# Performance work log

Hardware: AMD Instinct MI355X
Metric: run time of the kernel (lower is better)

## Reference

```python
import jax, jax.numpy as jnp
import numpy as np
from jax import lax

NUM_WORDS, WORD_DIM = 50000, 300
NUM_CHARS, CHAR_DIM = 100, 100
NUM_POS, POS_DIM = 50, 100
NUM_FILTERS, KERNEL = 100, 3
PRIVACY_TERMS = (3, 7, 11)


def setup_inputs() -> dict:
    key = jax.random.key(0)
    ks = jax.random.split(key, 8)
    bs, ls, cl = 64, 512, 32
    return {
        "input_word": jax.random.randint(ks[0], (bs, ls), 0, NUM_WORDS, dtype=jnp.int64 if jax.config.jax_enable_x64 else jnp.int32),
        "input_char": jax.random.randint(ks[1], (bs, ls, cl), 0, NUM_CHARS),
        "input_pos": jax.random.randint(ks[2], (bs, ls), 0, NUM_POS),
        "word_table": jax.random.normal(ks[3], (NUM_WORDS, WORD_DIM), jnp.float32) * 0.1,
        "char_table": jax.random.normal(ks[4], (NUM_CHARS, CHAR_DIM), jnp.float32) * 0.1,
        "pos_table": jax.random.normal(ks[5], (NUM_POS, POS_DIM), jnp.float32) * 0.1,
        "conv_w": jax.random.normal(ks[6], (NUM_FILTERS, CHAR_DIM, KERNEL), jnp.float32) * 0.05,
        "conv_b": jax.random.normal(ks[7], (NUM_FILTERS,), jnp.float32) * 0.05,
    }


def _dist_feature(input_pos):
    # nearest-privacy-token distance: parallel prefix-min via cummax/cummin scans
    priv = jnp.asarray(PRIVACY_TERMS)
    pri_mask = (input_pos[..., None] == priv).any(-1)           # [bs, ls]
    ls = input_pos.shape[1]
    pos_idx = jnp.arange(ls)                                      # [ls]
    last = lax.cummax(jnp.where(pri_mask, pos_idx, -1000), axis=1)                 # last privacy idx <= j
    nxt = lax.cummin(jnp.where(pri_mask, pos_idx, 1000), axis=1, reverse=True)     # next privacy idx >= j
    dis = jnp.minimum(pos_idx - last, nxt - pos_idx).astype(jnp.float32)
    return dis[..., None]                                         # [bs, ls, 1]


def _char_cnn(char_emb, conv_w, conv_b):
    # char_emb: [bs, ls, cl, char_dim] -> [bs, ls, num_filters]
    bs, ls, cl, cd = char_emb.shape
    x = char_emb.reshape(bs * ls, cl, cd).transpose(0, 2, 1)      # [N, C, L]
    y = lax.conv_general_dilated(x, conv_w, window_strides=(1,),
                                 padding=[(KERNEL - 1, KERNEL - 1)],
                                 dimension_numbers=("NCH", "OIH", "NCH"))
    y = y + conv_b[None, :, None]
    y = jnp.tanh(y.max(axis=2))                                   # max over length, then tanh
    return y.reshape(bs, ls, -1)


def reference(input_word, input_char, input_pos, word_table, char_table, pos_table, conv_w, conv_b):
    dis = _dist_feature(input_pos)
    word = word_table[input_word]                                 # [bs, ls, word_dim]
    char = _char_cnn(char_table[input_char], conv_w, conv_b)      # [bs, ls, num_filters]
    pos = pos_table[input_pos]                                    # [bs, ls, pos_dim]
    return jnp.concatenate([dis, word, char, pos], axis=2)
```

## Files before the change

### kernel.cpp

```cpp
#include <hip/hip_runtime.h>
#include <hip/hip_fp16.h>

#define BS 64
#define LS 512
#define CL 32
#define WD 300
#define NC 100
#define CD 100
#define PD 100
#define NF 100
#define KK 3
#define OPAD 128
#define PROW (KK*OPAD)
#define PBYTES (NC*PROW*2)
#define NV4 (PBYTES/16)
#define OUTD 501
#define TPB 64
#define NTHR 1024

typedef _Float16 h2 __attribute__((ext_vector_type(2)));

__global__ void precompute_P(const float* __restrict__ conv_w,
                             const float* __restrict__ char_table,
                             _Float16* __restrict__ P) {
    const int c = blockIdx.x;
    const int k = blockIdx.y;
    const int o = threadIdx.x;
    __shared__ float row[CD];
    if (o < CD) row[o] = char_table[c * CD + o];
    __syncthreads();
    float acc = 0.f;
    if (o < NF) {
        const float* w = conv_w + o * (CD * KK) + k;
        #pragma unroll 4
        for (int i = 0; i < CD; ++i) acc += w[i * KK] * row[i];
    }
    P[(c * KK + k) * OPAD + o] = (_Float16)acc;
}

__global__ __launch_bounds__(NTHR, 8) void main_kernel(
        const int* __restrict__ input_word,
        const int* __restrict__ input_char,
        const int* __restrict__ input_pos,
        const float* __restrict__ word_table,
        const float* __restrict__ pos_table,
        const float* __restrict__ conv_b,
        const _Float16* __restrict__ Pg,
        float* __restrict__ out) {
    __shared__ alignas(16) _Float16 Pl[NC * PROW];
    __shared__ alignas(16) unsigned char s_char[TPB * CL];
    __shared__ unsigned long long s_mask[LS / 64];

    const int tid  = threadIdx.x;
    const int tok0 = blockIdx.x * TPB;

    const uint4* src = (const uint4*)Pg;
    const uint4 s0 = src[tid];
    const uint4 s1 = src[tid + NTHR];
    const uint4 s2 = src[tid + 2 * NTHR];
    const uint4 s3 = src[tid + 3 * NTHR];
    uint4 s4 = {};
    const bool h4 = tid < (NV4 - 4 * NTHR);
    if (h4) s4 = src[tid + 4 * NTHR];

    if (tid < LS) {
        const int p = input_pos[(tok0 >> 9) * LS + tid];
        const bool pm = (p == 3) | (p == 7) | (p == 11);
        const unsigned long long b = __ballot(pm);
        if ((tid & 63) == 0) s_mask[tid >> 6] = b;
    }

    if (tid < (TPB * CL) / 4) {
        const int4 c4 = ((const int4*)(input_char + tok0 * CL))[tid];
        ((unsigned*)s_char)[tid] =
            (unsigned)c4.x | ((unsigned)c4.y << 8) | ((unsigned)c4.z << 16) | ((unsigned)c4.w << 24);
    }

    {
        uint4* dst = (uint4*)Pl;
        dst[tid] = s0;
        dst[tid + NTHR] = s1;
        dst[tid + 2 * NTHR] = s2;
        dst[tid + 3 * NTHR] = s3;
        if (h4) dst[tid + 4 * NTHR] = s4;
    }
    __syncthreads();

    if (tid < 512) {
        const int wid  = tid >> 6;
        const int lane = tid & 63;
        const int l    = lane & 15;
        const char* Pb = (const char*)Pl + l * 16;
        const unsigned* s_cw = (const unsigned*)s_char;

        #pragma unroll 1
        for (int pass = 0; pass < 2; ++pass) {
            const int tb = wid * 8 + pass * 4 + (lane >> 4);
            h2 a0[4], a1[4], m[4];
            #pragma unroll
            for (int i = 0; i < 4; ++i) {
                a0[i] = (h2)(_Float16)0;
                a1[i] = (h2)(_Float16)0;
                m[i]  = (h2)(_Float16)(-60000.f);
            }
            #pragma unroll 2
            for (int w = 0; w < CL / 4; ++w) {
                const unsigned wd = s_cw[tb * (CL / 4) + w];
                #pragma unroll
                for (int b = 0; b < 4; ++b) {
                    const int ca = (int)((wd >> (8 * b)) & 0xFFu) * (PROW * 2);
                    const uint4 r0 = *(const uint4*)(Pb + ca + 0 * (OPAD * 2));
                    const uint4 r1 = *(const uint4*)(Pb + ca + 1 * (OPAD * 2));
                    const uint4 r2 = *(const uint4*)(Pb + ca + 2 * (OPAD * 2));
                    #pragma unroll
                    for (int i = 0; i < 4; ++i) {
                        const unsigned c0 = (i == 0) ? r0.x : (i == 1) ? r0.y : (i == 2) ? r0.z : r0.w;
                        const unsigned c1 = (i == 0) ? r1.x : (i == 1) ? r1.y : (i == 2) ? r1.z : r1.w;
                        const unsigned c2 = (i == 0) ? r2.x : (i == 1) ? r2.y : (i == 2) ? r2.z : r2.w;
                        const h2 p0 = __builtin_bit_cast(h2, c0);
                        const h2 p1 = __builtin_bit_cast(h2, c1);
                        const h2 p2 = __builtin_bit_cast(h2, c2);
                        const h2 y = a0[i] + p2;
                        m[i]  = __builtin_elementwise_max(m[i], y);
                        a0[i] = a1[i] + p1;
                        a1[i] = p0;
                    }
                }
            }
            if (l < 13) {
                float mm[8];
                #pragma unroll
                for (int i = 0; i < 4; ++i) {
                    const h2 v = __builtin_elementwise_max(m[i], __builtin_elementwise_max(a0[i], a1[i]));
                    mm[2 * i]     = (float)v.x;
                    mm[2 * i + 1] = (float)v.y;
                }
                const float4 b0 = *(const float4*)(conv_b + 8 * l);
                float* outc = out + (size_t)(tok0 + tb) * OUTD + 301 + 8 * l;
                outc[0] = tanhf(mm[0] + b0.x);
                outc[1] = tanhf(mm[1] + b0.y);
                outc[2] = tanhf(mm[2] + b0.z);
                outc[3] = tanhf(mm[3] + b0.w);
                if (l < 12) {
                    const float4 b1 = *(const float4*)(conv_b + 8 * l + 4);
                    outc[4] = tanhf(mm[4] + b1.x);
                    outc[5] = tanhf(mm[5] + b1.y);
                    outc[6] = tanhf(mm[6] + b1.z);
                    outc[7] = tanhf(mm[7] + b1.w);
                }
            }
        }
    } else {
        const int t2 = tid - 512;

        for (int i = t2; i < TPB * (WD / 4); i += 512) {
            const int t = i / (WD / 4);
            const int j = i - t * (WD / 4);
            const int w = input_word[tok0 + t];
            const float4 v = ((const float4*)word_table)[(size_t)w * (WD / 4) + j];
            float* o = out + (size_t)(tok0 + t) * OUTD + 1 + 4 * j;
            o[0] = v.x; o[1] = v.y; o[2] = v.z; o[3] = v.w;
        }
        for (int i = t2; i < TPB * (PD / 4); i += 512) {
            const int t = i / (PD / 4);
            const int j = i - t * (PD / 4);
            const int p = input_pos[tok0 + t];
            const float4 v = ((const float4*)pos_table)[p * (PD / 4) + j];
            float* o = out + (size_t)(tok0 + t) * OUTD + 401 + 4 * j;
            o[0] = v.x; o[1] = v.y; o[2] = v.z; o[3] = v.w;
        }
        if (t2 < TPB) {
            const int j = (tok0 & (LS - 1)) + t2;
            const int wj = j >> 6, bj = j & 63;
            int last = -1000;
            {
                unsigned long long x = s_mask[wj] & ((2ull << bj) - 1ull);
                int w = wj;
                while (true) {
                    if (x) { last = w * 64 + 63 - __clzll(x); break; }
                    if (--w < 0) break;
                    x = s_mask[w];
                }
            }
            int nxt = 1000;
            {
                unsigned long long x = s_mask[wj] & (~0ull << bj);
                int w = wj;
                while (true) {
                    if (x) { nxt = w * 64 + (int)__ffsll((long long)x) - 1; break; }
                    if (++w >= LS / 64) break;
                    x = s_mask[w];
                }
            }
            out[(size_t)(tok0 + t2) * OUTD] = (float)min(j - last, nxt - j);
        }
    }
}

extern "C" void kernel_launch(void* const* d_in, const int* in_sizes, int n_in,
                              void* d_out, int out_size, void* d_ws, size_t ws_size,
                              hipStream_t stream) {
    const int*   input_word = (const int*)d_in[0];
    const int*   input_char = (const int*)d_in[1];
    const int*   input_pos  = (const int*)d_in[2];
    const float* word_table = (const float*)d_in[3];
    const float* char_table = (const float*)d_in[4];
    const float* pos_table  = (const float*)d_in[5];
    const float* conv_w     = (const float*)d_in[6];
    const float* conv_b     = (const float*)d_in[7];
    float* out = (float*)d_out;

    _Float16* P = (_Float16*)d_ws;

    precompute_P<<<dim3(NC, KK), 128, 0, stream>>>(conv_w, char_table, P);
    main_kernel<<<(BS * LS) / TPB, NTHR, 0, stream>>>(
        input_word, input_char, input_pos, word_table, pos_table, conv_b, P, out);
}
```

Baseline: 38.90 us.

## Store char-conv projection table in FP8 and rebalance gather work across halves

The precomputed char-by-filter projection table is now quantized to FP8 (e4m3) instead of FP16. This halves the table's global-to-LDS copy and the per-character LDS reads, with a packed fp8-to-f32-to-f16 conversion added in the inner loop. The pos-embedding gather and distance feature move from the word-gather half of the block to the CNN half, and the word-gather loop is unrolled. FP8 quantization of the conv partial sums adds significant numerical error that may exceed tolerance, and the extra conversion instructions add ALU cost.

```diff
diff --git a/kernel.cpp b/kernel.cpp
--- a/kernel.cpp
+++ b/kernel.cpp
@@ -10,19 +10,26 @@
 #define PD 100
 #define NF 100
 #define KK 3
-#define OPAD 128
-#define PROW (KK*OPAD)
-#define PBYTES (NC*PROW*2)
-#define NV4 (PBYTES/16)
+#define OPAD8 128
+#define PROW8 (KK*OPAD8)
+#define PBYTES8 (NC*PROW8)
+#define NV4_8 (PBYTES8/16)
 #define OUTD 501
 #define TPB 64
 #define NTHR 1024
 
 typedef _Float16 h2 __attribute__((ext_vector_type(2)));
+typedef float f32x2 __attribute__((ext_vector_type(2)));
+
+template <bool HI>
+__device__ __forceinline__ h2 cvt2(unsigned w) {
+    f32x2 f = __builtin_amdgcn_cvt_pk_f32_fp8((int)w, HI);
+    return __builtin_bit_cast(h2, __builtin_amdgcn_cvt_pkrtz(f.x, f.y));
+}
 
 __global__ void precompute_P(const float* __restrict__ conv_w,
                              const float* __restrict__ char_table,
-                             _Float16* __restrict__ P) {
+                             unsigned char* __restrict__ P) {
     const int c = blockIdx.x;
     const int k = blockIdx.y;
     const int o = threadIdx.x;
@@ -35,8 +42,20 @@
         #pragma unroll 4
         for (int i = 0; i < CD; ++i) acc += w[i * KK] * row[i];
     }
-    P[(c * KK + k) * OPAD + o] = (_Float16)acc;
-}
+    const int enc = __builtin_amdgcn_cvt_pk_fp8_f32(acc, 0.f, 0, false);
+    P[(c * KK + k) * OPAD8 + o] = (unsigned char)(enc & 0xFF);
+}
+
+#define TAP(i, W0, W1, W2, HI)                                          \
+    {                                                                   \
+        const h2 p0 = cvt2<HI>(W0);                                     \
+        const h2 p1 = cvt2<HI>(W1);                                     \
+        const h2 p2 = cvt2<HI>(W2);                                     \
+        const h2 y = a0[i] + p2;                                        \
+        m[i]  = __builtin_elementwise_max(m[i], y);                     \
+        a0[i] = a1[i] + p1;                                             \
+        a1[i] = p0;                                                     \
+    }
 
 __global__ __launch_bounds__(NTHR, 8) void main_kernel(
         const int* __restrict__ input_word,
@@ -45,9 +64,9 @@
         const float* __restrict__ word_table,
         const float* __restrict__ pos_table,
         const float* __restrict__ conv_b,
-        const _Float16* __restrict__ Pg,
+        const unsigned char* __restrict__ Pg,
         float* __restrict__ out) {
-    __shared__ alignas(16) _Float16 Pl[NC * PROW];
+    __shared__ alignas(16) unsigned char Pl[PBYTES8];
     __shared__ alignas(16) unsigned char s_char[TPB * CL];
     __shared__ unsigned long long s_mask[LS / 64];
 
@@ -57,11 +76,9 @@
     const uint4* src = (const uint4*)Pg;
     const uint4 s0 = src[tid];
     const uint4 s1 = src[tid + NTHR];
-    const uint4 s2 = src[tid + 2 * NTHR];
-    const uint4 s3 = src[tid + 3 * NTHR];
-    uint4 s4 = {};
-    const bool h4 = tid < (NV4 - 4 * NTHR);
-    if (h4) s4 = src[tid + 4 * NTHR];
+    uint4 s2 = {};
+    const bool h2nd = tid < (NV4_8 - 2 * NTHR);
+    if (h2nd) s2 = src[tid + 2 * NTHR];
 
     if (tid < LS) {
         const int p = input_pos[(tok0 >> 9) * LS + tid];
@@ -80,9 +97,7 @@
         uint4* dst = (uint4*)Pl;
         dst[tid] = s0;
         dst[tid + NTHR] = s1;
-        dst[tid + 2 * NTHR] = s2;
-        dst[tid + 3 * NTHR] = s3;
-        if (h4) dst[tid + 4 * NTHR] = s4;
+        if (h2nd) dst[tid + 2 * NTHR] = s2;
     }
     __syncthreads();
 
@@ -90,7 +105,7 @@
         const int wid  = tid >> 6;
         const int lane = tid & 63;
         const int l    = lane & 15;
-        const char* Pb = (const char*)Pl + l * 16;
+        const char* Pb = (const char*)Pl + l * 8;
         const unsigned* s_cw = (const unsigned*)s_char;
 
         #pragma unroll 1
@@ -103,28 +118,19 @@
                 a1[i] = (h2)(_Float16)0;
                 m[i]  = (h2)(_Float16)(-60000.f);
             }
-            #pragma unroll 2
+            #pragma unroll 1
             for (int w = 0; w < CL / 4; ++w) {
                 const unsigned wd = s_cw[tb * (CL / 4) + w];
                 #pragma unroll
                 for (int b = 0; b < 4; ++b) {
-                    const int ca = (int)((wd >> (8 * b)) & 0xFFu) * (PROW * 2);
-                    const uint4 r0 = *(const uint4*)(Pb + ca + 0 * (OPAD * 2));
-                    const uint4 r1 = *(const uint4*)(Pb + ca + 1 * (OPAD * 2));
-                    const uint4 r2 = *(const uint4*)(Pb + ca + 2 * (OPAD * 2));
-                    #pragma unroll
-                    for (int i = 0; i < 4; ++i) {
-                        const unsigned c0 = (i == 0) ? r0.x : (i == 1) ? r0.y : (i == 2) ? r0.z : r0.w;
-                        const unsigned c1 = (i == 0) ? r1.x : (i == 1) ? r1.y : (i == 2) ? r1.z : r1.w;
-                        const unsigned c2 = (i == 0) ? r2.x : (i == 1) ? r2.y : (i == 2) ? r2.z : r2.w;
-                        const h2 p0 = __builtin_bit_cast(h2, c0);
-                        const h2 p1 = __builtin_bit_cast(h2, c1);
-                        const h2 p2 = __builtin_bit_cast(h2, c2);
-                        const h2 y = a0[i] + p2;
-                        m[i]  = __builtin_elementwise_max(m[i], y);
-                        a0[i] = a1[i] + p1;
-                        a1[i] = p0;
-                    }
+                    const int ca = (int)((wd >> (8 * b)) & 0xFFu) * PROW8;
+                    const uint2 q0 = *(const uint2*)(Pb + ca + 0 * OPAD8);
+                    const uint2 q1 = *(const uint2*)(Pb + ca + 1 * OPAD8);
+                    const uint2 q2 = *(const uint2*)(Pb + ca + 2 * OPAD8);
+                    TAP(0, q0.x, q1.x, q2.x, false)
+                    TAP(1, q0.x, q1.x, q2.x, true)
+                    TAP(2, q0.y, q1.y, q2.y, false)
+                    TAP(3, q0.y, q1.y, q2.y, true)
                 }
             }
             if (l < 13) {
@@ -150,18 +156,8 @@
                 }
             }
         }
-    } else {
-        const int t2 = tid - 512;
-
-        for (int i = t2; i < TPB * (WD / 4); i += 512) {
-            const int t = i / (WD / 4);
-            const int j = i - t * (WD / 4);
-            const int w = input_word[tok0 + t];
-            const float4 v = ((const float4*)word_table)[(size_t)w * (WD / 4) + j];
-            float* o = out + (size_t)(tok0 + t) * OUTD + 1 + 4 * j;
-            o[0] = v.x; o[1] = v.y; o[2] = v.z; o[3] = v.w;
-        }
-        for (int i = t2; i < TPB * (PD / 4); i += 512) {
+
+        for (int i = tid; i < TPB * (PD / 4); i += 512) {
             const int t = i / (PD / 4);
             const int j = i - t * (PD / 4);
             const int p = input_pos[tok0 + t];
@@ -169,8 +165,9 @@
             float* o = out + (size_t)(tok0 + t) * OUTD + 401 + 4 * j;
             o[0] = v.x; o[1] = v.y; o[2] = v.z; o[3] = v.w;
         }
-        if (t2 < TPB) {
-            const int j = (tok0 & (LS - 1)) + t2;
+
+        if (tid < TPB) {
+            const int j = (tok0 & (LS - 1)) + tid;
             const int wj = j >> 6, bj = j & 63;
             int last = -1000;
             {
@@ -192,7 +189,19 @@
                     x = s_mask[w];
                 }
             }
-            out[(size_t)(tok0 + t2) * OUTD] = (float)min(j - last, nxt - j);
+            out[(size_t)(tok0 + tid) * OUTD] = (float)min(j - last, nxt - j);
+        }
+    } else {
+        const int t2 = tid - 512;
+
+        #pragma unroll 4
+        for (int i = t2; i < TPB * (WD / 4); i += 512) {
+            const int t = i / (WD / 4);
+            const int j = i - t * (WD / 4);
+            const int w = input_word[tok0 + t];
+            const float4 v = ((const float4*)word_table)[(size_t)w * (WD / 4) + j];
+            float* o = out + (size_t)(tok0 + t) * OUTD + 1 + 4 * j;
+            o[0] = v.x; o[1] = v.y; o[2] = v.z; o[3] = v.w;
         }
     }
 }
@@ -210,7 +219,7 @@
     const float* conv_b     = (const float*)d_in[7];
     float* out = (float*)d_out;
 
-    _Float16* P = (_Float16*)d_ws;
+    unsigned char* P = (unsigned char*)d_ws;
 
     precompute_P<<<dim3(NC, KK), 128, 0, stream>>>(conv_w, char_table, P);
     main_kernel<<<(BS * LS) / TPB, NTHR, 0, stream>>>(
```

New measurement: 44.52 us. +14.4%, slower.
